# Kernel tuning notes

Hardware: AMD Instinct MI355X
Metric: run time of the kernel (lower is better)

The kernel has to match this reference:

```python
import jax, jax.numpy as jnp
import numpy as np

TEMP_LEN = 16
TARGET_LEN = 22
NUM_HEADS = 16
DIM = 512
B = 16
N = TEMP_LEN**2 + TARGET_LEN**2  # 740


def bias_index(w_len, h_len):
    # Swin-style relative position index, matches torch getBiasIndex
    coords = jnp.stack(jnp.meshgrid(jnp.arange(h_len), jnp.arange(w_len), indexing='ij'))  # [2,h,w]
    flat = coords.reshape(2, -1)                       # [2, L]
    rel = flat[:, :, None] - flat[:, None, :]          # [2, L, L]
    rel = rel.transpose(1, 2, 0)                       # [L, L, 2]
    r0 = (rel[..., 0] + w_len - 1) * (2 * w_len - 1)
    r1 = rel[..., 1] + h_len - 1
    return r0 + r1                                     # [L, L] int32


def setup_inputs() -> dict:
    key = jax.random.key(0)
    ks = jax.random.split(key, 12)
    C, H = DIM, NUM_HEADS
    s = 0.0002
    return {
        'x': jax.random.normal(ks[0], (B, N, C), jnp.float32),
        'W_qkv': jax.random.normal(ks[1], (C, 3 * C), jnp.float32) * (1.0 / np.sqrt(C)),
        'b_qkv': jnp.zeros((3 * C,), jnp.float32),
        'W_proj': jax.random.normal(ks[2], (C, C), jnp.float32) * (1.0 / np.sqrt(C)),
        'b_proj': jnp.zeros((C,), jnp.float32),
        'bias_table_target': jax.random.normal(ks[3], ((2 * TARGET_LEN - 1) ** 2, H), jnp.float32) * s,
        'bias_table_temp': jax.random.normal(ks[4], ((2 * TEMP_LEN - 1) ** 2, H), jnp.float32) * s,
        'temp_target_table': jax.random.normal(ks[5], (H, TARGET_LEN**2, 1), jnp.float32) * s,
        'target_temp_table': jax.random.normal(ks[6], (H, TEMP_LEN**2, 1), jnp.float32) * s,
        'temp_target_line': jax.random.normal(ks[7], (H, 1, TEMP_LEN**2), jnp.float32) * s,
        'target_temp_line': jax.random.normal(ks[8], (H, 1, TARGET_LEN**2), jnp.float32) * s,
    }


def reference(x, W_qkv, b_qkv, W_proj, b_proj,
              bias_table_target, bias_table_temp,
              temp_target_table, target_temp_table,
              temp_target_line, target_temp_line):
    Bb, Nn, C = x.shape
    H = NUM_HEADS
    hd = C // H
    scale = hd ** -0.5

    qkv = (x @ W_qkv + b_qkv).reshape(Bb, Nn, 3, H, hd).transpose(2, 0, 3, 1, 4)
    q, k, v = qkv[0], qkv[1], qkv[2]  # each [B, H, N, hd]

    # --- relative position bias, concat of 4 blocks -> [H, N, N] ---
    idx_temp = bias_index(TEMP_LEN, TEMP_LEN)        # [256, 256]
    idx_target = bias_index(TARGET_LEN, TARGET_LEN)  # [484, 484]
    temp_bias = bias_table_temp[idx_temp].transpose(2, 0, 1)      # [H, 256, 256]
    target_bias = bias_table_target[idx_target].transpose(2, 0, 1)  # [H, 484, 484]
    temp_target = temp_target_table + temp_target_line            # [H, 484, 256]
    target_temp = target_temp_table + target_temp_line            # [H, 256, 484]
    left = jnp.concatenate([temp_bias, temp_target], axis=1)      # [H, 740, 256]
    right = jnp.concatenate([target_temp, target_bias], axis=1)   # [H, 740, 484]
    bias = jnp.concatenate([left, right], axis=2)                 # [H, 740, 740]

    attn = jnp.einsum('bhqd,bhkd->bhqk', q, k) * scale + bias[None]
    attn = jax.nn.softmax(attn, axis=-1)
    out = jnp.einsum('bhqk,bhkd->bhqd', attn, v)                  # [B, H, N, hd]
    out = out.transpose(0, 2, 1, 3).reshape(Bb, Nn, C)
    return out @ W_proj + b_proj
```

## Files before the change

### kernel.cpp

```cpp
#include <hip/hip_runtime.h>
#include <hip/hip_bf16.h>
#include <hip/hip_fp16.h>
#include <stdint.h>
#include <stddef.h>

typedef __attribute__((ext_vector_type(8))) short short8;
typedef __attribute__((ext_vector_type(4))) float f32x4;
typedef __attribute__((ext_vector_type(2))) float f32x2;
typedef unsigned short ushort_t;

#define NHEADS 16
#define HD 32
#define NQ 740
#define NB 16
#define MROWS (NB*NQ)
#define CD 512
#define KDIM 512
#define VSTRIDE 768
#define NQT 48
#define PTS 40
#define QS2 0.2550400865f
#define LOG2E 1.4426950409f
#define NEG_BIG -43000.0f

static __device__ __forceinline__ void gld_lds16(const void* g, void* l) {
    __builtin_amdgcn_global_load_lds((const __attribute__((address_space(1))) void*)g,
                                     (__attribute__((address_space(3))) void*)l,
                                     16, 0, 0);
}

static __device__ __forceinline__ float ldf(const void* p, int i, int fl) {
    return fl ? ((const float*)p)[i] : (float)((const __hip_bfloat16*)p)[i];
}
static __device__ __forceinline__ ushort_t f2bf(float f) {
    __hip_bfloat16 h(f);
    return *reinterpret_cast<ushort_t*>(&h);
}
static __device__ __forceinline__ float fexp2(float x) {
#if __has_builtin(__builtin_amdgcn_exp2f)
    return __builtin_amdgcn_exp2f(x);
#else
    return exp2f(x);
#endif
}
static __device__ __forceinline__ unsigned int f2e5(float f) {
    __half h = __float2half(f);
    unsigned short hb = *reinterpret_cast<unsigned short*>(&h);
    return (((unsigned int)hb + 0x7fu + ((hb >> 8) & 1u)) >> 8) & 0xffu;
}
#if __has_builtin(__builtin_amdgcn_cvt_pk_f32_bf8)
static __device__ __forceinline__ f32x4 bias4f8(unsigned int b) {
    f32x2 lo = __builtin_amdgcn_cvt_pk_f32_bf8((int)b, false);
    f32x2 hi = __builtin_amdgcn_cvt_pk_f32_bf8((int)b, true);
    f32x4 c;
    c[0] = lo[0]; c[1] = lo[1]; c[2] = hi[0]; c[3] = hi[1];
    return c;
}
#else
static __device__ __forceinline__ f32x4 bias4f8(unsigned int b) {
    f32x4 c;
    #pragma unroll
    for (int i = 0; i < 4; ++i) {
        union { unsigned short u; __half h; } cv;
        cv.u = (unsigned short)(((b >> (8 * i)) & 0xffu) << 8);
        c[i] = __half2float(cv.h);
    }
    return c;
}
#endif
static __device__ __forceinline__ void pkstore(__hip_bfloat16* dst, f32x4 c) {
    __hip_bfloat162* d = (__hip_bfloat162*)dst;
    d[0] = __float22bfloat162_rn(make_float2(c[0], c[1]));
    d[1] = __float22bfloat162_rn(make_float2(c[2], c[3]));
}
static __device__ __forceinline__ uint2 pk4(float a, float b, float c, float d) {
    __hip_bfloat162 p01 = __float22bfloat162_rn(make_float2(a, b));
    __hip_bfloat162 p23 = __float22bfloat162_rn(make_float2(c, d));
    uint2 u;
    u.x = *reinterpret_cast<unsigned int*>(&p01);
    u.y = *reinterpret_cast<unsigned int*>(&p23);
    return u;
}

__global__ __launch_bounds__(64) void sniff_k(const unsigned int* __restrict__ w,
                                              int* __restrict__ flag) {
    int cnt = 0;
    for (int i = threadIdx.x; i < 1024; i += 64) {
        unsigned int e = (w[i] >> 7) & 0xFFu;
        cnt += (e > 135u) ? 1 : 0;
    }
    #pragma unroll
    for (int d = 1; d < 64; d <<= 1) cnt += __shfl_xor(cnt, d);
    if (threadIdx.x == 0) *flag = (cnt > 16) ? 1 : 0;
}

#define PREP_CONV 1480
#define PREP_TA   768
#define PREP_TB   256
#define PREP_BIAS 768
__global__ __launch_bounds__(256) void prep_k(
    const void* __restrict__ x, ushort4* __restrict__ Xb,
    const void* __restrict__ Wqkv, __hip_bfloat16* __restrict__ WqT,
    const void* __restrict__ Wproj, __hip_bfloat16* __restrict__ WpT,
    const void* __restrict__ btT, const void* __restrict__ btt,
    const void* __restrict__ ttab, const void* __restrict__ tgtab,
    const void* __restrict__ ttln, const void* __restrict__ tgln,
    unsigned int* __restrict__ biasF,
    const int* __restrict__ flag) {
    __shared__ __hip_bfloat16 tile[32][33];
    const int bid = blockIdx.x;
    const int tid = threadIdx.x;
    const int fl = *flag;

    if (bid < PREP_CONV) {
        const int n = MROWS * CD / 4;
        for (int i = bid * 256 + tid; i < n; i += PREP_CONV * 256) {
            if (fl) {
                float4 v = ((const float4*)x)[i];
                ushort4 o;
                o.x = f2bf(v.x); o.y = f2bf(v.y); o.z = f2bf(v.z); o.w = f2bf(v.w);
                Xb[i] = o;
            } else {
                Xb[i] = ((const ushort4*)x)[i];
            }
        }
        return;
    }
    if (bid < PREP_CONV + PREP_TA + PREP_TB) {
        const void* src; __hip_bfloat16* dst; int R, C, lb;
        if (bid < PREP_CONV + PREP_TA) {
            src = Wqkv; dst = WqT; R = 512; C = 1536; lb = bid - PREP_CONV;
        } else {
            src = Wproj; dst = WpT; R = 512; C = 512; lb = bid - PREP_CONV - PREP_TA;
        }
        int nbx = C / 32;
        int bx = (lb % nbx) * 32;
        int by = (lb / nbx) * 32;
        int tx = tid & 31, ty = tid >> 5;
        for (int r = ty; r < 32; r += 8)
            tile[r][tx] = __hip_bfloat16(ldf(src, (by + r) * C + bx + tx, fl));
        __syncthreads();
        for (int r = ty; r < 32; r += 8)
            dst[(size_t)(bx + r) * R + by + tx] = tile[tx][r];
        return;
    }
    const int blk = bid - (PREP_CONV + PREP_TA + PREP_TB);
    const int hh = blk / NQT;
    const int qt = blk - hh * NQT;
    for (int idx = tid; idx < 48 * 64; idx += 256) {
        const int lane = idx & 63;
        const int kb = idx >> 6;
        const int lr = lane & 15, kc = lane >> 4;
        int i = qt * 16 + lr; if (i > NQ - 1) i = NQ - 1;
        unsigned int pk = 0;
        #pragma unroll
        for (int r = 0; r < 4; ++r) {
            int c = kb * 16 + kc * 4 + r;
            float v;
            if (c >= NQ) {
                v = NEG_BIG;
            } else if (i < 256) {
                if (c < 256) {
                    int t = ((i >> 4) - (c >> 4) + 15) * 31 + ((i & 15) - (c & 15) + 15);
                    v = ldf(btt, t * 16 + hh, fl) * LOG2E;
                } else {
                    v = (ldf(tgtab, hh * 256 + i, fl) + ldf(tgln, hh * 484 + (c - 256), fl)) * LOG2E;
                }
            } else {
                int ii = i - 256;
                if (c < 256) {
                    v = (ldf(ttab, hh * 484 + ii, fl) + ldf(ttln, hh * 256 + c, fl)) * LOG2E;
                } else {
                    int jj = c - 256;
                    int a = ii / 22, b2 = ii - a * 22;
                    int a2 = jj / 22, b3 = jj - a2 * 22;
                    int t = (a - a2 + 21) * 43 + (b2 - b3 + 21);
                    v = ldf(btT, t * 16 + hh, fl) * LOG2E;
                }
            }
            pk |= f2e5(v) << (8 * r);
        }
        biasF[(size_t)blk * 48 * 64 + idx] = pk;
    }
}

__global__ __launch_bounds__(256) void gemm_qkv(
    const __hip_bfloat16* __restrict__ A,
    const __hip_bfloat16* __restrict__ Bt,
    const void* __restrict__ biasv,
    __hip_bfloat16* __restrict__ Qw,
    __hip_bfloat16* __restrict__ Kw,
    __hip_bfloat16* __restrict__ Vtw,
    const int* __restrict__ flag) {
    __shared__ __attribute__((aligned(16))) short sStage[3 * 12288];
    const int tid = threadIdx.x;
    const int lane = tid & 63;
    const int wv = tid >> 6;
    const int lr = lane & 15, kc = lane >> 4;
    const int m0 = blockIdx.y * 256;
    const int n0 = blockIdx.x * 128;
    const int fl = *flag;
    const int M = MROWS;

    auto stage = [&](int s) {
        char* bb = (char*)sStage + (s % 3) * 24576;
        const int k0 = s * 32;
        #pragma unroll
        for (int it = 0; it < 6; ++it) {
            int idx = it * 256 + tid;
            if (idx < 1024) {
                int r = idx >> 2, c = idx & 3;
                int gr = m0 + r; if (gr > M - 1) gr = M - 1;
                gld_lds16(A + (size_t)gr * KDIM + k0 + c * 8, bb + idx * 16);
            } else {
                int u = idx - 1024;
                int r = u >> 2, c = u & 3;
                gld_lds16(Bt + (size_t)(n0 + r) * KDIM + k0 + c * 8, bb + 16384 + u * 16);
            }
        }
    };

    f32x4 acc[4][8] = {};
    stage(0);
    stage(1);

    for (int ks = 0; ks < 16; ++ks) {
        asm volatile("" ::: "memory");
        if (ks < 15) __builtin_amdgcn_s_waitcnt(0x0076);
        else         __builtin_amdgcn_s_waitcnt(0x0070);
        __builtin_amdgcn_s_barrier();
        asm volatile("" ::: "memory");
        if (ks + 2 < 16) stage(ks + 2);

        const char* bb = (const char*)sStage + (ks % 3) * 24576;
        const short* cA = (const short*)bb;
        const short* cB = (const short*)(bb + 16384);
        short8 af[4], bfr[8];
        #pragma unroll
        for (int t = 0; t < 4; ++t)
            af[t] = *(const short8*)&cA[(wv * 64 + t * 16 + lr) * 32 + kc * 8];
        #pragma unroll
        for (int t = 0; t < 8; ++t)
            bfr[t] = *(const short8*)&cB[(t * 16 + lr) * 32 + kc * 8];
        #pragma unroll
        for (int i = 0; i < 4; ++i)
            #pragma unroll
            for (int j = 0; j < 8; ++j)
                acc[i][j] = __builtin_amdgcn_mfma_f32_16x16x32_bf16(af[i], bfr[j], acc[i][j], 0, 0, 0);
    }

    const int s = n0 >> 9;
    short* Tw = (short*)((char*)sStage + 24576) + wv * 2560;
    const int gmr = m0 + wv * 64 + lane;
    int gmrc = gmr < M ? gmr : M - 1;
    int bq = gmrc / NQ;
    int nnq = gmrc - bq * NQ;
    const int gmv = m0 + wv * 64 + (lane & 15) * 4;
    int gmvc = gmv < M ? gmv : M - 1;
    int bv2 = gmvc / NQ;
    int nnv = gmvc - bv2 * NQ;

    #pragma unroll
    for (int t = 0; t < 4; ++t) {
        const int hh = ((n0 >> 5) + t) & 15;
        float bva = ldf(biasv, n0 + t * 32 + lr, fl);
        float bvb = ldf(biasv, n0 + t * 32 + 16 + lr, fl);
        asm volatile("" ::: "memory");
        if (s == 2) {
            #pragma unroll
            for (int i = 0; i < 4; ++i) {
                int nl = i * 16 + kc * 4;
                uint2 ua = pk4(acc[i][2*t][0] + bva, acc[i][2*t][1] + bva,
                               acc[i][2*t][2] + bva, acc[i][2*t][3] + bva);
                uint2 ub = pk4(acc[i][2*t+1][0] + bvb, acc[i][2*t+1][1] + bvb,
                               acc[i][2*t+1][2] + bvb, acc[i][2*t+1][3] + bvb);
                *(uint2*)(void*)&Tw[lr * 72 + nl]        = ua;
                *(uint2*)(void*)&Tw[(16 + lr) * 72 + nl] = ub;
            }
        } else {
            float sc = (s == 0) ? QS2 : 1.0f;
            #pragma unroll
            for (int i = 0; i < 4; ++i)
                #pragma unroll
                for (int r = 0; r < 4; ++r) {
                    int nl = i * 16 + kc * 4 + r;
                    Tw[nl * 40 + lr]      = (short)f2bf((acc[i][2*t][r]   + bva) * sc);
                    Tw[nl * 40 + 16 + lr] = (short)f2bf((acc[i][2*t+1][r] + bvb) * sc);
                }
        }
        asm volatile("" ::: "memory");
        __builtin_amdgcn_s_waitcnt(0xc07f);
        asm volatile("" ::: "memory");
        if (s == 2) {
            if (gmv < M) {
                size_t bh = (size_t)(bv2 * 16 + hh);
                #pragma unroll
                for (int i2 = 0; i2 < 8; ++i2) {
                    int d = (lane >> 4) + i2 * 4;
                    uint2 u = *(const uint2*)(const void*)&Tw[d * 72 + (lane & 15) * 4];
                    *(uint2*)(void*)(Vtw + (bh * HD + d) * VSTRIDE + nnv) = u;
                }
            }
        } else {
            if (gmr < M) {
                size_t bh = (size_t)(bq * 16 + hh);
                __hip_bfloat16* dst = (s == 0 ? Qw : Kw) + (bh * NQ + nnq) * HD;
                #pragma unroll
                for (int c = 0; c < 4; ++c) {
                    short8 u = *(const short8*)(const void*)&Tw[lane * 40 + c * 8];
                    *(short8*)(void*)(dst + c * 8) = u;
                }
            }
        }
        asm volatile("" ::: "memory");
        __builtin_amdgcn_s_waitcnt(0xc07f);
        asm volatile("" ::: "memory");
    }
}

__global__ __launch_bounds__(256) void gemm_bt(
    const __hip_bfloat16* __restrict__ A,
    const __hip_bfloat16* __restrict__ Bt,
    const void* __restrict__ biasv,
    int M,
    __hip_bfloat16* __restrict__ Out,
    float* __restrict__ OutF,
    const int* __restrict__ flag) {
    __shared__ __attribute__((aligned(16))) short sStage[3 * 8192];
    const int tid = threadIdx.x;
    const int lane = tid & 63;
    const int wv = tid >> 6;
    const int wr = wv >> 1, wc = wv & 1;
    const int lr = lane & 15, kc = lane >> 4;
    const int m0 = blockIdx.y * 128;
    const int n0 = blockIdx.x * 128;
    const int fl = *flag;

    auto stage = [&](int s) {
        char* bb = (char*)sStage + (s % 3) * 16384;
        const int k0 = s * 32;
        #pragma unroll
        for (int it = 0; it < 2; ++it) {
            int idx = it * 256 + tid;
            int r = idx >> 2;
            int c = idx & 3;
            int gr = m0 + r; if (gr > M - 1) gr = M - 1;
            gld_lds16(A + (size_t)gr * KDIM + k0 + c * 8, bb + idx * 16);
            gld_lds16(Bt + (size_t)(n0 + r) * KDIM + k0 + c * 8, bb + 8192 + idx * 16);
        }
    };

    f32x4 acc[4][4] = {};
    stage(0);
    stage(1);

    for (int ks = 0; ks < 16; ++ks) {
        asm volatile("" ::: "memory");
        if (ks < 15) __builtin_amdgcn_s_waitcnt(0x0074);
        else         __builtin_amdgcn_s_waitcnt(0x0070);
        __builtin_amdgcn_s_barrier();
        asm volatile("" ::: "memory");
        if (ks + 2 < 16) stage(ks + 2);

        const char* bb = (const char*)sStage + (ks % 3) * 16384;
        const short* cA = (const short*)bb;
        const short* cB = (const short*)(bb + 8192);
        short8 af[4], bfr[4];
        #pragma unroll
        for (int t = 0; t < 4; ++t)
            af[t] = *(const short8*)&cA[(wr * 64 + t * 16 + lr) * 32 + kc * 8];
        #pragma unroll
        for (int t = 0; t < 4; ++t)
            bfr[t] = *(const short8*)&cB[(wc * 64 + t * 16 + lr) * 32 + kc * 8];
        #pragma unroll
        for (int i = 0; i < 4; ++i)
            #pragma unroll
            for (int j = 0; j < 4; ++j)
                acc[i][j] = __builtin_amdgcn_mfma_f32_16x16x32_bf16(af[i], bfr[j], acc[i][j], 0, 0, 0);
    }

    #pragma unroll
    for (int i = 0; i < 4; ++i) {
        #pragma unroll
        for (int j = 0; j < 4; ++j) {
            int gn = n0 + wc * 64 + j * 16 + lr;
            float bv = ldf(biasv, gn, fl);
            #pragma unroll
            for (int r = 0; r < 4; ++r) {
                int gm = m0 + wr * 64 + i * 16 + kc * 4 + r;
                if (gm < M) {
                    float v = acc[i][j][r] + bv;
                    if (fl) OutF[(size_t)gm * CD + gn] = v;
                    else    Out[(size_t)gm * CD + gn] = __hip_bfloat16(v);
                }
            }
        }
    }
}

__global__ __launch_bounds__(256) void attn_k(
    const __hip_bfloat16* __restrict__ Qw,
    const __hip_bfloat16* __restrict__ Kw,
    const __hip_bfloat16* __restrict__ Vtw,
    const unsigned int* __restrict__ biasF,
    __hip_bfloat16* __restrict__ AO) {
    __shared__ __attribute__((aligned(16))) short sStage[3 * 2048];
    __shared__ __attribute__((aligned(16))) __hip_bfloat16 Pt[4][32 * PTS];

    const int tid = threadIdx.x;
    const int wv = tid >> 6;
    const int pair = blockIdx.x * 4 + wv;
    const int bh = blockIdx.y;
    const int hh = bh & 15;
    const int b = bh >> 4;
    const int q0 = pair * 32;
    const int lane = tid & 63;
    const int lr = lane & 15, kc = lane >> 4;

    const __hip_bfloat16* Qb = Qw + (size_t)bh * NQ * HD;
    const __hip_bfloat16* Kb = Kw + (size_t)bh * NQ * HD;
    const __hip_bfloat16* Vb = Vtw + (size_t)bh * HD * VSTRIDE;
    __hip_bfloat16* Pw = &Pt[wv][0];

    short8 qfA = *(const short8*)(const void*)(Qb + (q0 + lr) * HD + kc * 8);
    short8 qfB = *(const short8*)(const void*)(Qb + (q0 + 16 + lr) * HD + kc * 8);

    short8 onesf;
    {
        short s1 = (lr == 0) ? (short)0x3F80 : (short)0;
        #pragma unroll
        for (int j = 0; j < 8; ++j) onesf[j] = s1;
    }

    const unsigned int* bt0 = biasF + (size_t)(hh * NQT + 2 * pair) * 48 * 64 + lane;
    const unsigned int* bt1 = bt0 + 48 * 64;

    unsigned int brA0[2], brA1[2], brB0[2], brB1[2];
    brA0[0] = bt0[0];  brA1[0] = bt0[64];
    brB0[0] = bt1[0];  brB1[0] = bt1[64];

    {
        const void* src;
        if (tid < 128) src = Kb + (tid & 31) * HD + (tid >> 5) * 8;
        else { int u = tid - 128; src = Vb + (u & 31) * VSTRIDE + ((u >> 5) & 3) * 8; }
        gld_lds16(src, (char*)sStage + tid * 16);
    }
    asm volatile("" ::: "memory");

    f32x4 oa0 = {}, ob0 = {}, ol0 = {};
    f32x4 oa1 = {}, ob1 = {}, ol1 = {};

    #pragma unroll
    for (int ks = 0; ks < 24; ++ks) {
        const int cur = ks & 1, nxt = cur ^ 1;
        if (ks < 23) {
            brA0[nxt] = bt0[(2 * ks + 2) * 64];
            brA1[nxt] = bt0[(2 * ks + 3) * 64];
            brB0[nxt] = bt1[(2 * ks + 2) * 64];
            brB1[nxt] = bt1[(2 * ks + 3) * 64];
            const int k0n = (ks + 1) * 32;
            const int nb = ((ks + 1) % 3) * 4096;
            const void* src;
            if (tid < 128) src = Kb + (k0n + (tid & 31)) * HD + (tid >> 5) * 8;
            else { int u = tid - 128; src = Vb + (u & 31) * VSTRIDE + k0n + ((u >> 5) & 3) * 8; }
            gld_lds16(src, (char*)sStage + nb + tid * 16);
        }
        asm volatile("" ::: "memory");
        if (ks < 23) __builtin_amdgcn_s_waitcnt(0x0F75);
        else         __builtin_amdgcn_s_waitcnt(0x0F70);
        __builtin_amdgcn_s_barrier();
        asm volatile("" ::: "memory");

        const short* sK = (const short*)((const char*)sStage + (ks % 3) * 4096);
        const short* sV = sK + 1024;
        short8 kf0 = *(const short8*)&sK[kc * 256 + lr * 8];
        short8 kf1 = *(const short8*)&sK[kc * 256 + (16 + lr) * 8];
        short8 vf0 = *(const short8*)&sV[kc * 256 + lr * 8];
        short8 vf1 = *(const short8*)&sV[kc * 256 + (16 + lr) * 8];

        f32x4 c0 = bias4f8(brA0[cur]);
        f32x4 c1 = bias4f8(brA1[cur]);
        f32x4 c2 = bias4f8(brB0[cur]);
        f32x4 c3 = bias4f8(brB1[cur]);

        c0 = __builtin_amdgcn_mfma_f32_16x16x32_bf16(kf0, qfA, c0, 0, 0, 0);
        c1 = __builtin_amdgcn_mfma_f32_16x16x32_bf16(kf1, qfA, c1, 0, 0, 0);
        c2 = __builtin_amdgcn_mfma_f32_16x16x32_bf16(kf0, qfB, c2, 0, 0, 0);
        c3 = __builtin_amdgcn_mfma_f32_16x16x32_bf16(kf1, qfB, c3, 0, 0, 0);

        #pragma unroll
        for (int r = 0; r < 4; ++r) {
            c0[r] = fexp2(c0[r]); c1[r] = fexp2(c1[r]);
            c2[r] = fexp2(c2[r]); c3[r] = fexp2(c3[r]);
        }
        pkstore(Pw + lr * PTS + kc * 4, c0);
        pkstore(Pw + lr * PTS + 16 + kc * 4, c1);
        pkstore(Pw + (16 + lr) * PTS + kc * 4, c2);
        pkstore(Pw + (16 + lr) * PTS + 16 + kc * 4, c3);
        asm volatile("" ::: "memory");
        __builtin_amdgcn_s_waitcnt(0xc07f);
        asm volatile("" ::: "memory");

        short8 pfA = *(const short8*)(const void*)(Pw + lr * PTS + kc * 8);
        short8 pfB = *(const short8*)(const void*)(Pw + (16 + lr) * PTS + kc * 8);

        oa0 = __builtin_amdgcn_mfma_f32_16x16x32_bf16(pfA, vf0, oa0, 0, 0, 0);
        ob0 = __builtin_amdgcn_mfma_f32_16x16x32_bf16(pfA, vf1, ob0, 0, 0, 0);
        ol0 = __builtin_amdgcn_mfma_f32_16x16x32_bf16(pfA, onesf, ol0, 0, 0, 0);
        oa1 = __builtin_amdgcn_mfma_f32_16x16x32_bf16(pfB, vf0, oa1, 0, 0, 0);
        ob1 = __builtin_amdgcn_mfma_f32_16x16x32_bf16(pfB, vf1, ob1, 0, 0, 0);
        ol1 = __builtin_amdgcn_mfma_f32_16x16x32_bf16(pfB, onesf, ol1, 0, 0, 0);
    }

    #pragma unroll
    for (int r = 0; r < 4; ++r) {
        int row = kc * 4 + r;
        float lA = __shfl(ol0[r], lane & 48);
        float lB = __shfl(ol1[r], lane & 48);
        float liA = 1.0f / lA, liB = 1.0f / lB;
        int orA = q0 + row, orB = q0 + 16 + row;
        if (orA < NQ) {
            size_t base = ((size_t)b * NQ + orA) * CD + hh * HD;
            AO[base + lr]      = __hip_bfloat16(oa0[r] * liA);
            AO[base + 16 + lr] = __hip_bfloat16(ob0[r] * liA);
        }
        if (orB < NQ) {
            size_t base = ((size_t)b * NQ + orB) * CD + hh * HD;
            AO[base + lr]      = __hip_bfloat16(oa1[r] * liB);
            AO[base + 16 + lr] = __hip_bfloat16(ob1[r] * liB);
        }
    }
}

extern "C" void kernel_launch(void* const* d_in, const int* in_sizes, int n_in,
                              void* d_out, int out_size, void* d_ws, size_t ws_size,
                              hipStream_t stream) {
    char* ws = (char*)d_ws;
    size_t off = 0;
    auto carve = [&](size_t bytes) {
        char* p = ws + off;
        off += (bytes + 255) & ~(size_t)255;
        return p;
    };
    int* flagp = (int*)carve(256);
    __hip_bfloat16* Qw    = (__hip_bfloat16*)carve((size_t)256 * NQ * HD * 2);
    __hip_bfloat16* Kw    = (__hip_bfloat16*)carve((size_t)256 * NQ * HD * 2);
    __hip_bfloat16* Vtw   = (__hip_bfloat16*)carve((size_t)256 * HD * VSTRIDE * 2);
    __hip_bfloat16* WqT   = (__hip_bfloat16*)carve((size_t)1536 * 512 * 2);
    __hip_bfloat16* WpT   = (__hip_bfloat16*)carve((size_t)512 * 512 * 2);
    unsigned int*   biasF = (unsigned int*)carve((size_t)16 * NQT * 48 * 64 * 4);
    __hip_bfloat16* Xb    = (__hip_bfloat16*)carve((size_t)MROWS * CD * 2);
    __hip_bfloat16* AO    = Xb;
    (void)ws_size; (void)in_sizes; (void)n_in; (void)out_size;

    sniff_k<<<dim3(1), dim3(64), 0, stream>>>((const unsigned int*)d_in[1], flagp);
    prep_k<<<dim3(PREP_CONV + PREP_TA + PREP_TB + PREP_BIAS), dim3(256), 0, stream>>>(
        d_in[0], (ushort4*)Xb, d_in[1], WqT, d_in[3], WpT,
        d_in[5], d_in[6], d_in[7], d_in[8], d_in[9], d_in[10], biasF, flagp);
    gemm_qkv<<<dim3(12, 47), dim3(256), 0, stream>>>(Xb, WqT, d_in[2],
        Qw, Kw, Vtw, flagp);
    attn_k<<<dim3(6, 256), dim3(256), 0, stream>>>(Qw, Kw, Vtw, biasF, AO);
    gemm_bt<<<dim3(4, 93), dim3(256), 0, stream>>>(AO, WpT, d_in[4], MROWS,
        (__hip_bfloat16*)d_out, (float*)d_out, flagp);
}
```

Before: 221.1 us.

## Transpose P in registers via permlane swaps and deepen K/V prefetch

Replaces the LDS round-trip for the softmax probability tile (pack to bf16, store to shared memory, wait, reload as the MFMA A operand) with in-register cross-lane permutes using v_permlane32/16_swap. It also moves the K/V global-to-LDS prefetch after the barrier and issues it two steps ahead into the three-slot ring, with two tiles preloaded in the prologue. This removes per-wave LDS traffic and an lgkm wait from the inner loop, but the waitcnt thresholds were not adjusted for the deeper prefetch depth, which risks stalls or a correctness problem.

Result: no change. 225.5 us (+2.0%).

```diff
diff --git a/kernel.cpp b/kernel.cpp
--- a/kernel.cpp
+++ b/kernel.cpp
@@ -18,7 +18,6 @@
 #define KDIM 512
 #define VSTRIDE 768
 #define NQT 48
-#define PTS 40
 #define QS2 0.2550400865f
 #define LOG2E 1.4426950409f
 #define NEG_BIG -43000.0f
@@ -68,11 +67,6 @@
     return c;
 }
 #endif
-static __device__ __forceinline__ void pkstore(__hip_bfloat16* dst, f32x4 c) {
-    __hip_bfloat162* d = (__hip_bfloat162*)dst;
-    d[0] = __float22bfloat162_rn(make_float2(c[0], c[1]));
-    d[1] = __float22bfloat162_rn(make_float2(c[2], c[3]));
-}
 static __device__ __forceinline__ uint2 pk4(float a, float b, float c, float d) {
     __hip_bfloat162 p01 = __float22bfloat162_rn(make_float2(a, b));
     __hip_bfloat162 p23 = __float22bfloat162_rn(make_float2(c, d));
@@ -80,6 +74,23 @@
     u.x = *reinterpret_cast<unsigned int*>(&p01);
     u.y = *reinterpret_cast<unsigned int*>(&p23);
     return u;
+}
+static __device__ __forceinline__ unsigned int pkw(float a, float b) {
+    __hip_bfloat162 p = __float22bfloat162_rn(make_float2(a, b));
+    return *reinterpret_cast<unsigned int*>(&p);
+}
+static __device__ __forceinline__ void xpose4(unsigned int& w0, unsigned int& w1,
+                                              unsigned int& w2, unsigned int& w3) {
+    asm("v_permlane32_swap_b32 %0, %1" : "+v"(w0), "+v"(w2));
+    asm("v_permlane32_swap_b32 %0, %1" : "+v"(w1), "+v"(w3));
+    asm("v_permlane16_swap_b32 %0, %1" : "+v"(w0), "+v"(w2));
+    asm("v_permlane16_swap_b32 %0, %1" : "+v"(w1), "+v"(w3));
+}
+static __device__ __forceinline__ short8 mk8(unsigned int w0, unsigned int w1,
+                                             unsigned int w2, unsigned int w3) {
+    union { unsigned int u[4]; short8 s; } t;
+    t.u[0] = w0; t.u[1] = w1; t.u[2] = w2; t.u[3] = w3;
+    return t.s;
 }
 
 __global__ __launch_bounds__(64) void sniff_k(const unsigned int* __restrict__ w,
@@ -405,7 +416,6 @@
     const unsigned int* __restrict__ biasF,
     __hip_bfloat16* __restrict__ AO) {
     __shared__ __attribute__((aligned(16))) short sStage[3 * 2048];
-    __shared__ __attribute__((aligned(16))) __hip_bfloat16 Pt[4][32 * PTS];
 
     const int tid = threadIdx.x;
     const int wv = tid >> 6;
@@ -420,7 +430,6 @@
     const __hip_bfloat16* Qb = Qw + (size_t)bh * NQ * HD;
     const __hip_bfloat16* Kb = Kw + (size_t)bh * NQ * HD;
     const __hip_bfloat16* Vb = Vtw + (size_t)bh * HD * VSTRIDE;
-    __hip_bfloat16* Pw = &Pt[wv][0];
 
     short8 qfA = *(const short8*)(const void*)(Qb + (q0 + lr) * HD + kc * 8);
     short8 qfB = *(const short8*)(const void*)(Qb + (q0 + 16 + lr) * HD + kc * 8);
@@ -444,6 +453,9 @@
         if (tid < 128) src = Kb + (tid & 31) * HD + (tid >> 5) * 8;
         else { int u = tid - 128; src = Vb + (u & 31) * VSTRIDE + ((u >> 5) & 3) * 8; }
         gld_lds16(src, (char*)sStage + tid * 16);
+        if (tid < 128) src = Kb + (32 + (tid & 31)) * HD + (tid >> 5) * 8;
+        else { int u = tid - 128; src = Vb + (u & 31) * VSTRIDE + 32 + ((u >> 5) & 3) * 8; }
+        gld_lds16(src, (char*)sStage + 4096 + tid * 16);
     }
     asm volatile("" ::: "memory");
 
@@ -458,17 +470,20 @@
             brA1[nxt] = bt0[(2 * ks + 3) * 64];
             brB0[nxt] = bt1[(2 * ks + 2) * 64];
             brB1[nxt] = bt1[(2 * ks + 3) * 64];
-            const int k0n = (ks + 1) * 32;
-            const int nb = ((ks + 1) % 3) * 4096;
+        }
+        asm volatile("" ::: "memory");
+        if (ks < 23) __builtin_amdgcn_s_waitcnt(0x0F75);
+        else         __builtin_amdgcn_s_waitcnt(0x0F70);
+        __builtin_amdgcn_s_barrier();
+        asm volatile("" ::: "memory");
+        if (ks < 22) {
+            const int k0n = (ks + 2) * 32;
+            const int nb = ((ks + 2) % 3) * 4096;
             const void* src;
             if (tid < 128) src = Kb + (k0n + (tid & 31)) * HD + (tid >> 5) * 8;
             else { int u = tid - 128; src = Vb + (u & 31) * VSTRIDE + k0n + ((u >> 5) & 3) * 8; }
             gld_lds16(src, (char*)sStage + nb + tid * 16);
         }
-        asm volatile("" ::: "memory");
-        if (ks < 23) __builtin_amdgcn_s_waitcnt(0x0F75);
-        else         __builtin_amdgcn_s_waitcnt(0x0F70);
-        __builtin_amdgcn_s_barrier();
         asm volatile("" ::: "memory");
 
         const short* sK = (const short*)((const char*)sStage + (ks % 3) * 4096);
@@ -493,16 +508,15 @@
             c0[r] = fexp2(c0[r]); c1[r] = fexp2(c1[r]);
             c2[r] = fexp2(c2[r]); c3[r] = fexp2(c3[r]);
         }
-        pkstore(Pw + lr * PTS + kc * 4, c0);
-        pkstore(Pw + lr * PTS + 16 + kc * 4, c1);
-        pkstore(Pw + (16 + lr) * PTS + kc * 4, c2);
-        pkstore(Pw + (16 + lr) * PTS + 16 + kc * 4, c3);
-        asm volatile("" ::: "memory");
-        __builtin_amdgcn_s_waitcnt(0xc07f);
-        asm volatile("" ::: "memory");
-
-        short8 pfA = *(const short8*)(const void*)(Pw + lr * PTS + kc * 8);
-        short8 pfB = *(const short8*)(const void*)(Pw + (16 + lr) * PTS + kc * 8);
+
+        unsigned int a0 = pkw(c0[0], c0[1]), a1 = pkw(c0[2], c0[3]);
+        unsigned int a2 = pkw(c1[0], c1[1]), a3 = pkw(c1[2], c1[3]);
+        unsigned int e0 = pkw(c2[0], c2[1]), e1 = pkw(c2[2], c2[3]);
+        unsigned int e2 = pkw(c3[0], c3[1]), e3 = pkw(c3[2], c3[3]);
+        xpose4(a0, a1, a2, a3);
+        xpose4(e0, e1, e2, e3);
+        short8 pfA = mk8(a0, a1, a2, a3);
+        short8 pfB = mk8(e0, e1, e2, e3);
 
         oa0 = __builtin_amdgcn_mfma_f32_16x16x32_bf16(pfA, vf0, oa0, 0, 0, 0);
         ob0 = __builtin_amdgcn_mfma_f32_16x16x32_bf16(pfA, vf1, ob0, 0, 0, 0);
```

## Process 64 query rows per wave in attention to amortize K/V loads

Applied to the files above, without the earlier changes.

Each wave in the attention kernel now handles 64 query rows instead of 32, so the grid shrinks from 6 to 3 blocks along the query dimension. Each K/V tile staged in shared memory is reused across twice as many queries, halving K/V global traffic and barrier/staging overhead per query. The cost is more registers, a larger P scratch buffer in shared memory, and fewer blocks (768 vs 1536), which may reduce occupancy and latency hiding. Launch bounds and the wait count are adjusted for the extra bias loads in flight.

Result: faster. 215.5 us (-2.6%).

```diff
diff --git a/kernel.cpp b/kernel.cpp
--- a/kernel.cpp
+++ b/kernel.cpp
@@ -398,22 +398,22 @@
     }
 }
 
-__global__ __launch_bounds__(256) void attn_k(
+__global__ __launch_bounds__(256, 3) void attn_k(
     const __hip_bfloat16* __restrict__ Qw,
     const __hip_bfloat16* __restrict__ Kw,
     const __hip_bfloat16* __restrict__ Vtw,
     const unsigned int* __restrict__ biasF,
     __hip_bfloat16* __restrict__ AO) {
     __shared__ __attribute__((aligned(16))) short sStage[3 * 2048];
-    __shared__ __attribute__((aligned(16))) __hip_bfloat16 Pt[4][32 * PTS];
+    __shared__ __attribute__((aligned(16))) __hip_bfloat16 Pt[4][64 * PTS];
 
     const int tid = threadIdx.x;
     const int wv = tid >> 6;
-    const int pair = blockIdx.x * 4 + wv;
+    const int p = blockIdx.x * 4 + wv;
     const int bh = blockIdx.y;
     const int hh = bh & 15;
     const int b = bh >> 4;
-    const int q0 = pair * 32;
+    const int q0 = p * 64;
     const int lane = tid & 63;
     const int lr = lane & 15, kc = lane >> 4;
 
@@ -424,6 +424,8 @@
 
     short8 qfA = *(const short8*)(const void*)(Qb + (q0 + lr) * HD + kc * 8);
     short8 qfB = *(const short8*)(const void*)(Qb + (q0 + 16 + lr) * HD + kc * 8);
+    short8 qfC = *(const short8*)(const void*)(Qb + (q0 + 32 + lr) * HD + kc * 8);
+    short8 qfD = *(const short8*)(const void*)(Qb + (q0 + 48 + lr) * HD + kc * 8);
 
     short8 onesf;
     {
@@ -432,12 +434,17 @@
         for (int j = 0; j < 8; ++j) onesf[j] = s1;
     }
 
-    const unsigned int* bt0 = biasF + (size_t)(hh * NQT + 2 * pair) * 48 * 64 + lane;
+    const unsigned int* bt0 = biasF + (size_t)(hh * NQT + 4 * p) * 48 * 64 + lane;
     const unsigned int* bt1 = bt0 + 48 * 64;
+    const unsigned int* bt2 = bt0 + 2 * 48 * 64;
+    const unsigned int* bt3 = bt0 + 3 * 48 * 64;
 
     unsigned int brA0[2], brA1[2], brB0[2], brB1[2];
+    unsigned int brC0[2], brC1[2], brD0[2], brD1[2];
     brA0[0] = bt0[0];  brA1[0] = bt0[64];
     brB0[0] = bt1[0];  brB1[0] = bt1[64];
+    brC0[0] = bt2[0];  brC1[0] = bt2[64];
+    brD0[0] = bt3[0];  brD1[0] = bt3[64];
 
     {
         const void* src;
@@ -449,6 +456,8 @@
 
     f32x4 oa0 = {}, ob0 = {}, ol0 = {};
     f32x4 oa1 = {}, ob1 = {}, ol1 = {};
+    f32x4 oa2 = {}, ob2 = {}, ol2 = {};
+    f32x4 oa3 = {}, ob3 = {}, ol3 = {};
 
     #pragma unroll
     for (int ks = 0; ks < 24; ++ks) {
@@ -458,6 +467,10 @@
             brA1[nxt] = bt0[(2 * ks + 3) * 64];
             brB0[nxt] = bt1[(2 * ks + 2) * 64];
             brB1[nxt] = bt1[(2 * ks + 3) * 64];
+            brC0[nxt] = bt2[(2 * ks + 2) * 64];
+            brC1[nxt] = bt2[(2 * ks + 3) * 64];
+            brD0[nxt] = bt3[(2 * ks + 2) * 64];
+            brD1[nxt] = bt3[(2 * ks + 3) * 64];
             const int k0n = (ks + 1) * 32;
             const int nb = ((ks + 1) % 3) * 4096;
             const void* src;
@@ -466,7 +479,7 @@
             gld_lds16(src, (char*)sStage + nb + tid * 16);
         }
         asm volatile("" ::: "memory");
-        if (ks < 23) __builtin_amdgcn_s_waitcnt(0x0F75);
+        if (ks < 23) __builtin_amdgcn_s_waitcnt(0x0F79);
         else         __builtin_amdgcn_s_waitcnt(0x0F70);
         __builtin_amdgcn_s_barrier();
         asm volatile("" ::: "memory");
@@ -478,31 +491,56 @@
         short8 vf0 = *(const short8*)&sV[kc * 256 + lr * 8];
         short8 vf1 = *(const short8*)&sV[kc * 256 + (16 + lr) * 8];
 
-        f32x4 c0 = bias4f8(brA0[cur]);
-        f32x4 c1 = bias4f8(brA1[cur]);
-        f32x4 c2 = bias4f8(brB0[cur]);
-        f32x4 c3 = bias4f8(brB1[cur]);
-
-        c0 = __builtin_amdgcn_mfma_f32_16x16x32_bf16(kf0, qfA, c0, 0, 0, 0);
-        c1 = __builtin_amdgcn_mfma_f32_16x16x32_bf16(kf1, qfA, c1, 0, 0, 0);
-        c2 = __builtin_amdgcn_mfma_f32_16x16x32_bf16(kf0, qfB, c2, 0, 0, 0);
-        c3 = __builtin_amdgcn_mfma_f32_16x16x32_bf16(kf1, qfB, c3, 0, 0, 0);
-
-        #pragma unroll
-        for (int r = 0; r < 4; ++r) {
-            c0[r] = fexp2(c0[r]); c1[r] = fexp2(c1[r]);
-            c2[r] = fexp2(c2[r]); c3[r] = fexp2(c3[r]);
-        }
-        pkstore(Pw + lr * PTS + kc * 4, c0);
-        pkstore(Pw + lr * PTS + 16 + kc * 4, c1);
-        pkstore(Pw + (16 + lr) * PTS + kc * 4, c2);
-        pkstore(Pw + (16 + lr) * PTS + 16 + kc * 4, c3);
+        {
+            f32x4 c0 = bias4f8(brA0[cur]);
+            f32x4 c1 = bias4f8(brA1[cur]);
+            f32x4 c2 = bias4f8(brB0[cur]);
+            f32x4 c3 = bias4f8(brB1[cur]);
+
+            c0 = __builtin_amdgcn_mfma_f32_16x16x32_bf16(kf0, qfA, c0, 0, 0, 0);
+            c1 = __builtin_amdgcn_mfma_f32_16x16x32_bf16(kf1, qfA, c1, 0, 0, 0);
+            c2 = __builtin_amdgcn_mfma_f32_16x16x32_bf16(kf0, qfB, c2, 0, 0, 0);
+            c3 = __builtin_amdgcn_mfma_f32_16x16x32_bf16(kf1, qfB, c3, 0, 0, 0);
+
+            #pragma unroll
+            for (int r = 0; r < 4; ++r) {
+                c0[r] = fexp2(c0[r]); c1[r] = fexp2(c1[r]);
+                c2[r] = fexp2(c2[r]); c3[r] = fexp2(c3[r]);
+            }
+            pkstore(Pw + lr * PTS + kc * 4, c0);
+            pkstore(Pw + lr * PTS + 16 + kc * 4, c1);
+            pkstore(Pw + (16 + lr) * PTS + kc * 4, c2);
+            pkstore(Pw + (16 + lr) * PTS + 16 + kc * 4, c3);
+        }
+        {
+            f32x4 c0 = bias4f8(brC0[cur]);
+            f32x4 c1 = bias4f8(brC1[cur]);
+            f32x4 c2 = bias4f8(brD0[cur]);
+            f32x4 c3 = bias4f8(brD1[cur]);
+
+            c0 = __builtin_amdgcn_mfma_f32_16x16x32_bf16(kf0, qfC, c0, 0, 0, 0);
+            c1 = __builtin_amdgcn_mfma_f32_16x16x32_bf16(kf1, qfC, c1, 0, 0, 0);
+            c2 = __builtin_amdgcn_mfma_f32_16x16x32_bf16(kf0, qfD, c2, 0, 0, 0);
+            c3 = __builtin_amdgcn_mfma_f32_16x16x32_bf16(kf1, qfD, c3, 0, 0, 0);
+
+            #pragma unroll
+            for (int r = 0; r < 4; ++r) {
+                c0[r] = fexp2(c0[r]); c1[r] = fexp2(c1[r]);
+                c2[r] = fexp2(c2[r]); c3[r] = fexp2(c3[r]);
+            }
+            pkstore(Pw + (32 + lr) * PTS + kc * 4, c0);
+            pkstore(Pw + (32 + lr) * PTS + 16 + kc * 4, c1);
+            pkstore(Pw + (48 + lr) * PTS + kc * 4, c2);
+            pkstore(Pw + (48 + lr) * PTS + 16 + kc * 4, c3);
+        }
         asm volatile("" ::: "memory");
         __builtin_amdgcn_s_waitcnt(0xc07f);
         asm volatile("" ::: "memory");
 
         short8 pfA = *(const short8*)(const void*)(Pw + lr * PTS + kc * 8);
         short8 pfB = *(const short8*)(const void*)(Pw + (16 + lr) * PTS + kc * 8);
+        short8 pfC = *(const short8*)(const void*)(Pw + (32 + lr) * PTS + kc * 8);
+        short8 pfD = *(const short8*)(const void*)(Pw + (48 + lr) * PTS + kc * 8);
 
         oa0 = __builtin_amdgcn_mfma_f32_16x16x32_bf16(pfA, vf0, oa0, 0, 0, 0);
         ob0 = __builtin_amdgcn_mfma_f32_16x16x32_bf16(pfA, vf1, ob0, 0, 0, 0);
@@ -510,6 +548,12 @@
         oa1 = __builtin_amdgcn_mfma_f32_16x16x32_bf16(pfB, vf0, oa1, 0, 0, 0);
         ob1 = __builtin_amdgcn_mfma_f32_16x16x32_bf16(pfB, vf1, ob1, 0, 0, 0);
         ol1 = __builtin_amdgcn_mfma_f32_16x16x32_bf16(pfB, onesf, ol1, 0, 0, 0);
+        oa2 = __builtin_amdgcn_mfma_f32_16x16x32_bf16(pfC, vf0, oa2, 0, 0, 0);
+        ob2 = __builtin_amdgcn_mfma_f32_16x16x32_bf16(pfC, vf1, ob2, 0, 0, 0);
+        ol2 = __builtin_amdgcn_mfma_f32_16x16x32_bf16(pfC, onesf, ol2, 0, 0, 0);
+        oa3 = __builtin_amdgcn_mfma_f32_16x16x32_bf16(pfD, vf0, oa3, 0, 0, 0);
+        ob3 = __builtin_amdgcn_mfma_f32_16x16x32_bf16(pfD, vf1, ob3, 0, 0, 0);
+        ol3 = __builtin_amdgcn_mfma_f32_16x16x32_bf16(pfD, onesf, ol3, 0, 0, 0);
     }
 
     #pragma unroll
@@ -517,8 +561,12 @@
         int row = kc * 4 + r;
         float lA = __shfl(ol0[r], lane & 48);
         float lB = __shfl(ol1[r], lane & 48);
+        float lC = __shfl(ol2[r], lane & 48);
+        float lD = __shfl(ol3[r], lane & 48);
         float liA = 1.0f / lA, liB = 1.0f / lB;
+        float liC = 1.0f / lC, liD = 1.0f / lD;
         int orA = q0 + row, orB = q0 + 16 + row;
+        int orC = q0 + 32 + row, orD = q0 + 48 + row;
         if (orA < NQ) {
             size_t base = ((size_t)b * NQ + orA) * CD + hh * HD;
             AO[base + lr]      = __hip_bfloat16(oa0[r] * liA);
@@ -528,6 +576,16 @@
             size_t base = ((size_t)b * NQ + orB) * CD + hh * HD;
             AO[base + lr]      = __hip_bfloat16(oa1[r] * liB);
             AO[base + 16 + lr] = __hip_bfloat16(ob1[r] * liB);
+        }
+        if (orC < NQ) {
+            size_t base = ((size_t)b * NQ + orC) * CD + hh * HD;
+            AO[base + lr]      = __hip_bfloat16(oa2[r] * liC);
+            AO[base + 16 + lr] = __hip_bfloat16(ob2[r] * liC);
+        }
+        if (orD < NQ) {
+            size_t base = ((size_t)b * NQ + orD) * CD + hh * HD;
+            AO[base + lr]      = __hip_bfloat16(oa3[r] * liD);
+            AO[base + 16 + lr] = __hip_bfloat16(ob3[r] * liD);
         }
     }
 }
@@ -559,7 +617,7 @@
         d_in[5], d_in[6], d_in[7], d_in[8], d_in[9], d_in[10], biasF, flagp);
     gemm_qkv<<<dim3(12, 47), dim3(256), 0, stream>>>(Xb, WqT, d_in[2],
         Qw, Kw, Vtw, flagp);
-    attn_k<<<dim3(6, 256), dim3(256), 0, stream>>>(Qw, Kw, Vtw, biasF, AO);
+    attn_k<<<dim3(3, 256), dim3(256), 0, stream>>>(Qw, Kw, Vtw, biasF, AO);
     gemm_bt<<<dim3(4, 93), dim3(256), 0, stream>>>(AO, WpT, d_in[4], MROWS,
         (__hip_bfloat16*)d_out, (float*)d_out, flagp);
 }
```
